# Kernel tuning notes

Hardware: AMD Instinct MI355X
Metric: run time of the kernel (lower is better)

Reference implementation:

```python
import jax, jax.numpy as jnp
import numpy as np

N_EMBD = 1024
N_HEAD = 16
R = 16
SCALING = 1.0 / 16.0  # loralib default lora_alpha=1, scaling = alpha/r


def lora_linear(x, W, b, A, B):
    # loralib: y = x @ W.T + b + (x @ A.T) @ B.T * scaling
    return x @ W.T + b + (x @ A.T) @ B.T * SCALING


def setup_inputs() -> dict:
    key = jax.random.key(0)
    ks = jax.random.split(key, 16)
    B, T, S, C = 8, 1024, 256, N_EMBD
    std = 0.02
    return {
        "x": jax.random.normal(ks[0], (B, T, C), jnp.float32),
        "feature": jax.random.normal(ks[1], (B, S, C), jnp.float32),
        # c_attn (q projection)
        "Wq": jax.random.normal(ks[2], (C, C), jnp.float32) * std,
        "bq": jnp.zeros((C,), jnp.float32),
        "Aq": jax.random.normal(ks[3], (R, C), jnp.float32) * std,
        "Bq": jnp.zeros((C, R), jnp.float32),
        # feature_attn (kv projection)
        "Wf": jax.random.normal(ks[4], (2 * C, C), jnp.float32) * std,
        "bf": jnp.zeros((2 * C,), jnp.float32),
        "Af": jax.random.normal(ks[5], (R, C), jnp.float32) * std,
        "Bf": jnp.zeros((2 * C, R), jnp.float32),
        # c_proj
        "Wp": jax.random.normal(ks[6], (C, C), jnp.float32) * std,
        "bp": jnp.zeros((C,), jnp.float32),
        "Ap": jax.random.normal(ks[7], (R, C), jnp.float32) * std,
        "Bp": jnp.zeros((C, R), jnp.float32),
    }


def reference(x, feature, Wq, bq, Aq, Bq, Wf, bf, Af, Bf, Wp, bp, Ap, Bp):
    Bsz, T, C = x.shape
    S = feature.shape[1]
    H = N_HEAD
    D = C // H

    q = lora_linear(x, Wq, bq, Aq, Bq).reshape(Bsz, T, H, D).transpose(0, 2, 1, 3)
    kv = lora_linear(feature, Wf, bf, Af, Bf)
    k, v = kv[..., :C], kv[..., C:]
    k = k.reshape(Bsz, S, H, D).transpose(0, 2, 1, 3)
    v = v.reshape(Bsz, S, H, D).transpose(0, 2, 1, 3)

    att = jnp.einsum("bhtd,bhsd->bhts", q, k) * (1.0 / np.sqrt(D))
    mask = jnp.tril(jnp.ones((T, S), bool))  # bias[:, :, :T, :S]
    att = jnp.where(mask, att, -jnp.inf)
    att = jax.nn.softmax(att, axis=-1)

    y = jnp.einsum("bhts,bhsd->bhtd", att, v)
    y = y.transpose(0, 2, 1, 3).reshape(Bsz, T, C)
    return lora_linear(y, Wp, bp, Ap, Bp)
```

## Files before the change

kernel.cpp:

```cpp
#include <hip/hip_runtime.h>
#include <hip/hip_bf16.h>
#include <stdint.h>
#include <stddef.h>

typedef __hip_bfloat16 bf16;
typedef __attribute__((ext_vector_type(8))) short short8;
typedef __attribute__((ext_vector_type(4))) float floatx4;

__device__ __forceinline__ void async_load16(const bf16* g, bf16* l) {
#if defined(__has_builtin) && __has_builtin(__builtin_amdgcn_global_load_lds)
  __builtin_amdgcn_global_load_lds((__attribute__((address_space(1))) void*)g,
                                   (__attribute__((address_space(3))) void*)l,
                                   16, 0, 0);
#else
  *(short8*)l = *(const short8*)g;
#endif
}

__device__ __forceinline__ int wave_detect_f32(const unsigned short* __restrict__ xr) {
  const int lane = threadIdx.x & 63;
  const unsigned short u = xr[lane];
  const int e = (u >> 7) & 0xFF;
  const unsigned long long m = __ballot(e >= 0x93);
  return (__popcll(m) > 5) ? 1 : 0;
}

__device__ __forceinline__ float ldf(const void* p, int i, int flg) {
  return flg ? ((const float*)p)[i] : __bfloat162float(((const bf16*)p)[i]);
}

struct PrepArgs {
  const void *x, *ft, *bq, *bf, *bp;
  const void *Wq, *Aq, *Bq, *Wf, *Af, *Bf, *Wp, *Ap, *Bp;
  bf16 *cx, *cft, *cbq, *cbf, *cbp, *weffq, *wefff, *weffp;
};

__device__ __forceinline__ void canon4(const void* src, bf16* dst, int i4, int flg) {
  if (flg) {
    const float4 v = ((const float4*)src)[i4];
    dst[i4 * 4 + 0] = __float2bfloat16(v.x);
    dst[i4 * 4 + 1] = __float2bfloat16(v.y);
    dst[i4 * 4 + 2] = __float2bfloat16(v.z);
    dst[i4 * 4 + 3] = __float2bfloat16(v.w);
  } else {
    ((uint2*)dst)[i4] = ((const uint2*)src)[i4];
  }
}

__device__ __forceinline__ void weff1(const void* W, const void* Bm, const void* Am,
                                      bf16* dst, int idx, int flg) {
  const int n = idx >> 10, k = idx & 1023;
  float acc = 0.f;
#pragma unroll
  for (int r = 0; r < 16; ++r)
    acc += ldf(Bm, n * 16 + r, flg) * ldf(Am, r * 1024 + k, flg);
  dst[idx] = __float2bfloat16(ldf(W, idx, flg) + 0.0625f * acc);
}

__global__ __launch_bounds__(256) void prep_kernel(PrepArgs a) {
  const int flg = wave_detect_f32((const unsigned short*)a.x);
  const int bid = blockIdx.x, tid = threadIdx.x;
  if (bid < 8192) {
    canon4(a.x, a.cx, bid * 256 + tid, flg);
  } else if (bid < 10240) {
    canon4(a.ft, a.cft, (bid - 8192) * 256 + tid, flg);
  } else if (bid < 10241) {
    canon4(a.bq, a.cbq, tid, flg);
  } else if (bid < 10243) {
    canon4(a.bf, a.cbf, (bid - 10241) * 256 + tid, flg);
  } else if (bid < 10244) {
    canon4(a.bp, a.cbp, tid, flg);
  } else if (bid < 14340) {
    weff1(a.Wq, a.Bq, a.Aq, a.weffq, (bid - 10244) * 256 + tid, flg);
  } else if (bid < 22532) {
    weff1(a.Wf, a.Bf, a.Af, a.wefff, (bid - 14340) * 256 + tid, flg);
  } else {
    weff1(a.Wp, a.Bp, a.Ap, a.weffp, (bid - 22532) * 256 + tid, flg);
  }
}

__global__ __launch_bounds__(256) void gemm_qkv(
    const bf16* __restrict__ cx, const bf16* __restrict__ cft,
    const bf16* __restrict__ weffq, const bf16* __restrict__ wefff,
    const bf16* __restrict__ cbq, const bf16* __restrict__ cbf,
    bf16* __restrict__ qws, bf16* __restrict__ kws, bf16* __restrict__ vtws) {
  __shared__ __align__(16) bf16 sA[128 * 32];
  __shared__ __align__(16) bf16 sB[128 * 32];
  const int bid = blockIdx.x, tid = threadIdx.x;
  const int K = 1024;
  int mode, bm, bn;
  const bf16 *A, *Bt, *bias;
  if (bid < 512) {
    mode = 0; A = cx; Bt = weffq; bias = cbq;
    bm = (((bid & 7) << 3) | ((bid >> 3) & 7)) * 128;
    bn = (bid >> 6) * 128;
  } else {
    const int b2 = bid - 512;
    mode = 1; A = cft; Bt = wefff; bias = cbf;
    bm = (((b2 & 7) << 1) | ((b2 >> 3) & 1)) * 128;
    bn = (b2 >> 4) * 128;
  }
  const int srow = tid >> 2;
  const int scol = ((tid & 3) ^ (srow & 3)) << 3;
  const bf16* ga0 = A + (size_t)(bm + srow) * K + scol;
  const bf16* ga1 = ga0 + (size_t)64 * K;
  const bf16* gb0 = Bt + (size_t)(bn + srow) * K + scol;
  const bf16* gb1 = gb0 + (size_t)64 * K;
  bf16* lA0 = sA + tid * 8;
  bf16* lA1 = sA + 2048 + tid * 8;
  bf16* lB0 = sB + tid * 8;
  bf16* lB1 = sB + 2048 + tid * 8;
  const int wave = tid >> 6, lane = tid & 63;
  const int wm = (wave >> 1) << 6, wn = (wave & 1) << 6;
  const int lrow = lane & 15, quad = lane >> 4;
  const int swz = ((quad ^ (lrow & 3)) << 3);

  const floatx4 zero4 = {0.f, 0.f, 0.f, 0.f};
  floatx4 acc[4][4];
#pragma unroll
  for (int i = 0; i < 4; ++i)
#pragma unroll
    for (int j = 0; j < 4; ++j) acc[i][j] = zero4;

  for (int k0 = 0; k0 < K; k0 += 32) {
    async_load16(ga0, lA0);
    async_load16(ga1, lA1);
    async_load16(gb0, lB0);
    async_load16(gb1, lB1);
    ga0 += 32; ga1 += 32; gb0 += 32; gb1 += 32;
    __syncthreads();
    short8 af[4], bfr[4];
#pragma unroll
    for (int i = 0; i < 4; ++i) {
      af[i]  = *(const short8*)(sA + (wm + i * 16 + lrow) * 32 + swz);
      bfr[i] = *(const short8*)(sB + (wn + i * 16 + lrow) * 32 + swz);
    }
#pragma unroll
    for (int i = 0; i < 4; ++i)
#pragma unroll
      for (int j = 0; j < 4; ++j)
        acc[i][j] = __builtin_amdgcn_mfma_f32_16x16x32_bf16(af[i], bfr[j], acc[i][j], 0, 0, 0);
    __syncthreads();
  }

#pragma unroll
  for (int i = 0; i < 4; ++i) {
    const int mbase = bm + wm + i * 16 + quad * 4;
#pragma unroll
    for (int j = 0; j < 4; ++j) {
      const int n = bn + wn + j * 16 + lrow;
      const float bv = __bfloat162float(bias[n]);
#pragma unroll
      for (int r = 0; r < 4; ++r) {
        const int m = mbase + r;
        const bf16 hval = __float2bfloat16(acc[i][j][r] + bv);
        if (mode == 0) {
          const int b = m >> 10, t = m & 1023, hh = n >> 6, d = n & 63;
          qws[(((size_t)(b * 16 + hh)) * 1024 + t) * 64 + d] = hval;
        } else {
          const int b = m >> 8, s = m & 255;
          if (n < 1024) {
            const int hh = n >> 6, d = n & 63;
            kws[(((size_t)(b * 16 + hh)) * 256 + s) * 64 + d] = hval;
          } else {
            const int nn = n - 1024, hh = nn >> 6, d = nn & 63;
            vtws[(((size_t)(b * 16 + hh)) * 64 + d) * 256 + s] = hval;
          }
        }
      }
    }
  }
}

__global__ __launch_bounds__(256) void gemm_out(
    const bf16* __restrict__ A, const bf16* __restrict__ Bt,
    const bf16* __restrict__ bias, void* __restrict__ out0,
    const unsigned short* __restrict__ xraw) {
  __shared__ __align__(16) bf16 sA[128 * 32];
  __shared__ __align__(16) bf16 sB[128 * 32];
  const int bid = blockIdx.x, tid = threadIdx.x;
  const int K = 1024, N = 1024;
  const int bm = (((bid & 7) << 3) | ((bid >> 3) & 7)) * 128;
  const int bn = (bid >> 6) * 128;
  const int srow = tid >> 2;
  const int scol = ((tid & 3) ^ (srow & 3)) << 3;
  const bf16* ga0 = A + (size_t)(bm + srow) * K + scol;
  const bf16* ga1 = ga0 + (size_t)64 * K;
  const bf16* gb0 = Bt + (size_t)(bn + srow) * K + scol;
  const bf16* gb1 = gb0 + (size_t)64 * K;
  bf16* lA0 = sA + tid * 8;
  bf16* lA1 = sA + 2048 + tid * 8;
  bf16* lB0 = sB + tid * 8;
  bf16* lB1 = sB + 2048 + tid * 8;
  const int wave = tid >> 6, lane = tid & 63;
  const int wm = (wave >> 1) << 6, wn = (wave & 1) << 6;
  const int lrow = lane & 15, quad = lane >> 4;
  const int swz = ((quad ^ (lrow & 3)) << 3);

  const floatx4 zero4 = {0.f, 0.f, 0.f, 0.f};
  floatx4 acc[4][4];
#pragma unroll
  for (int i = 0; i < 4; ++i)
#pragma unroll
    for (int j = 0; j < 4; ++j) acc[i][j] = zero4;

  for (int k0 = 0; k0 < K; k0 += 32) {
    async_load16(ga0, lA0);
    async_load16(ga1, lA1);
    async_load16(gb0, lB0);
    async_load16(gb1, lB1);
    ga0 += 32; ga1 += 32; gb0 += 32; gb1 += 32;
    __syncthreads();
    short8 af[4], bfr[4];
#pragma unroll
    for (int i = 0; i < 4; ++i) {
      af[i]  = *(const short8*)(sA + (wm + i * 16 + lrow) * 32 + swz);
      bfr[i] = *(const short8*)(sB + (wn + i * 16 + lrow) * 32 + swz);
    }
#pragma unroll
    for (int i = 0; i < 4; ++i)
#pragma unroll
      for (int j = 0; j < 4; ++j)
        acc[i][j] = __builtin_amdgcn_mfma_f32_16x16x32_bf16(af[i], bfr[j], acc[i][j], 0, 0, 0);
    __syncthreads();
  }

  const int flg = wave_detect_f32(xraw);
#pragma unroll
  for (int i = 0; i < 4; ++i) {
    const int mbase = bm + wm + i * 16 + quad * 4;
#pragma unroll
    for (int j = 0; j < 4; ++j) {
      const int n = bn + wn + j * 16 + lrow;
      const float bv = __bfloat162float(bias[n]);
#pragma unroll
      for (int r = 0; r < 4; ++r) {
        const int m = mbase + r;
        const float fval = acc[i][j][r] + bv;
        const size_t idx = (size_t)m * N + n;
        if (flg) ((float*)out0)[idx] = fval;
        else     ((bf16*)out0)[idx] = __float2bfloat16(fval);
      }
    }
  }
}

#define SKP 72
#define SVP 264
__global__ __launch_bounds__(512, 2) void attn_kernel(
    const bf16* __restrict__ qws, const bf16* __restrict__ kws,
    const bf16* __restrict__ vtws, bf16* __restrict__ yws) {
  const int b = blockIdx.z, h = blockIdx.y, qc = blockIdx.x;
  const int bh = b * 16 + h;
  __shared__ __align__(16) bf16 sK[256 * SKP];
  __shared__ __align__(16) bf16 sVt[64 * SVP];
  __shared__ __align__(16) bf16 sP[8][16 * SVP];
  const int tid = threadIdx.x, wave = tid >> 6, lane = tid & 63;
  const int lrow = lane & 15, quad = lane >> 4;
  const bf16* kg = kws + (size_t)bh * (256 * 64);
  const bf16* vg = vtws + (size_t)bh * (64 * 256);
#pragma unroll
  for (int i = 0; i < 4; ++i) {
    const int idx = i * 512 + tid;
    const int kr = idx >> 3, kc = (idx & 7) * 8;
    *(short8*)(sK + kr * SKP + kc) = *(const short8*)(kg + kr * 64 + kc);
    const int vr = idx >> 5, vc = (idx & 31) * 8;
    *(short8*)(sVt + vr * SVP + vc) = *(const short8*)(vg + vr * 256 + vc);
  }
  __syncthreads();
  bf16* sPw = sP[wave];
  const floatx4 zero4 = {0.f, 0.f, 0.f, 0.f};
  const float kscale = 0.18033688011112042f;

  for (int st = 0; st < 4; ++st) {
    const int t0 = qc * 512 + wave * 64 + st * 16;
    const bf16* qrow = qws + ((size_t)bh * 1024 + t0 + lrow) * 64;
    const short8 aq0 = *(const short8*)(qrow + quad * 8);
    const short8 aq1 = *(const short8*)(qrow + 32 + quad * 8);
    floatx4 sc[16];
#pragma unroll
    for (int nt = 0; nt < 16; ++nt) {
      floatx4 c = zero4;
      c = __builtin_amdgcn_mfma_f32_16x16x32_bf16(
          aq0, *(const short8*)(sK + (nt * 16 + lrow) * SKP + quad * 8), c, 0, 0, 0);
      c = __builtin_amdgcn_mfma_f32_16x16x32_bf16(
          aq1, *(const short8*)(sK + (nt * 16 + lrow) * SKP + 32 + quad * 8), c, 0, 0, 0);
      sc[nt] = c;
    }
    float sum[4] = {0.f, 0.f, 0.f, 0.f};
#pragma unroll
    for (int nt = 0; nt < 16; ++nt) {
      const int s = nt * 16 + lrow;
#pragma unroll
      for (int r = 0; r < 4; ++r) {
        const int t = t0 + quad * 4 + r;
        const float p = (s <= t) ? exp2f(sc[nt][r] * kscale) : 0.f;
        sum[r] += p;
        sPw[(quad * 4 + r) * SVP + nt * 16 + lrow] = __float2bfloat16(p);
      }
    }
#pragma unroll
    for (int r = 0; r < 4; ++r) {
      sum[r] += __shfl_xor(sum[r], 1, 16);
      sum[r] += __shfl_xor(sum[r], 2, 16);
      sum[r] += __shfl_xor(sum[r], 4, 16);
      sum[r] += __shfl_xor(sum[r], 8, 16);
    }
    asm volatile("s_waitcnt lgkmcnt(0)" ::: "memory");
    floatx4 ya[4];
#pragma unroll
    for (int nt = 0; nt < 4; ++nt) ya[nt] = zero4;
#pragma unroll
    for (int ks = 0; ks < 8; ++ks) {
      const short8 ap = *(const short8*)(sPw + lrow * SVP + ks * 32 + quad * 8);
#pragma unroll
      for (int nt = 0; nt < 4; ++nt)
        ya[nt] = __builtin_amdgcn_mfma_f32_16x16x32_bf16(
            ap, *(const short8*)(sVt + (nt * 16 + lrow) * SVP + ks * 32 + quad * 8),
            ya[nt], 0, 0, 0);
    }
#pragma unroll
    for (int r = 0; r < 4; ++r) {
      const float rl = 1.f / sum[r];
      const int t = t0 + quad * 4 + r;
#pragma unroll
      for (int nt = 0; nt < 4; ++nt)
        yws[((size_t)b * 1024 + t) * 1024 + h * 64 + nt * 16 + lrow] =
            __float2bfloat16(ya[nt][r] * rl);
    }
  }
}

extern "C" void kernel_launch(void* const* d_in, const int* in_sizes, int n_in,
                              void* d_out, int out_size, void* d_ws, size_t ws_size,
                              hipStream_t stream) {
  char* p = (char*)d_ws;
  bf16* cbq   = (bf16*)p;     p += 4096;
  bf16* cbf   = (bf16*)p;     p += 8192;
  bf16* cbp   = (bf16*)p;     p += 4096;
  bf16* weffq = (bf16*)p;     p += (size_t)1024 * 1024 * 2;
  bf16* wefff = (bf16*)p;     p += (size_t)2048 * 1024 * 2;
  bf16* weffp = (bf16*)p;     p += (size_t)1024 * 1024 * 2;
  bf16* qws   = (bf16*)p;     p += (size_t)8 * 16 * 1024 * 64 * 2;
  bf16* kws   = (bf16*)p;     p += (size_t)8 * 16 * 256 * 64 * 2;
  bf16* vtws  = (bf16*)p;     p += (size_t)8 * 16 * 64 * 256 * 2;
  bf16* cft   = (bf16*)p;     p += (size_t)8 * 256 * 1024 * 2;
  bf16* cx    = (bf16*)p;     p += (size_t)8 * 1024 * 1024 * 2;
  bf16* yws   = cx;
  const size_t required = (size_t)(p - (char*)d_ws);
  if (ws_size < required) return;

  PrepArgs pa;
  pa.x = d_in[0]; pa.ft = d_in[1];
  pa.bq = d_in[3]; pa.bf = d_in[7]; pa.bp = d_in[11];
  pa.Wq = d_in[2];  pa.Aq = d_in[4];  pa.Bq = d_in[5];
  pa.Wf = d_in[6];  pa.Af = d_in[8];  pa.Bf = d_in[9];
  pa.Wp = d_in[10]; pa.Ap = d_in[12]; pa.Bp = d_in[13];
  pa.cx = cx; pa.cft = cft; pa.cbq = cbq; pa.cbf = cbf; pa.cbp = cbp;
  pa.weffq = weffq; pa.wefff = wefff; pa.weffp = weffp;
  prep_kernel<<<26628, 256, 0, stream>>>(pa);

  gemm_qkv<<<768, 256, 0, stream>>>(cx, cft, weffq, wefff, cbq, cbf, qws, kws, vtws);
  attn_kernel<<<dim3(2, 16, 8), 512, 0, stream>>>(qws, kws, vtws, yws);
  gemm_out<<<512, 256, 0, stream>>>(yws, weffp, cbp, d_out, (const unsigned short*)d_in[0]);
}
```

Baseline: 229.3 us.

## Double-buffer LDS tiles in QKV and output GEMMs with a single barrier

Both GEMM kernels now keep two LDS buffers per operand. The next K-tile's async global-to-LDS loads are issued right after the barrier, so they overlap with the MFMA work on the current tile, and the trailing __syncthreads per iteration is dropped. The XOR swizzle on LDS columns is also removed, so fragment reads use plain quad offsets. That may bring back LDS bank conflicts, and LDS use per block doubles, which can reduce occupancy.

Measured after the change: 237.5 us. 1.04x slower.

```diff
diff --git a/kernel.cpp b/kernel.cpp
--- a/kernel.cpp
+++ b/kernel.cpp
@@ -84,8 +84,8 @@
     const bf16* __restrict__ weffq, const bf16* __restrict__ wefff,
     const bf16* __restrict__ cbq, const bf16* __restrict__ cbf,
     bf16* __restrict__ qws, bf16* __restrict__ kws, bf16* __restrict__ vtws) {
-  __shared__ __align__(16) bf16 sA[128 * 32];
-  __shared__ __align__(16) bf16 sB[128 * 32];
+  __shared__ __align__(16) bf16 sA[2][128 * 32];
+  __shared__ __align__(16) bf16 sB[2][128 * 32];
   const int bid = blockIdx.x, tid = threadIdx.x;
   const int K = 1024;
   int mode, bm, bn;
@@ -100,20 +100,14 @@
     bm = (((b2 & 7) << 1) | ((b2 >> 3) & 1)) * 128;
     bn = (b2 >> 4) * 128;
   }
-  const int srow = tid >> 2;
-  const int scol = ((tid & 3) ^ (srow & 3)) << 3;
+  const int srow = tid >> 2, scol = (tid & 3) << 3;
   const bf16* ga0 = A + (size_t)(bm + srow) * K + scol;
   const bf16* ga1 = ga0 + (size_t)64 * K;
   const bf16* gb0 = Bt + (size_t)(bn + srow) * K + scol;
   const bf16* gb1 = gb0 + (size_t)64 * K;
-  bf16* lA0 = sA + tid * 8;
-  bf16* lA1 = sA + 2048 + tid * 8;
-  bf16* lB0 = sB + tid * 8;
-  bf16* lB1 = sB + 2048 + tid * 8;
   const int wave = tid >> 6, lane = tid & 63;
   const int wm = (wave >> 1) << 6, wn = (wave & 1) << 6;
   const int lrow = lane & 15, quad = lane >> 4;
-  const int swz = ((quad ^ (lrow & 3)) << 3);
 
   const floatx4 zero4 = {0.f, 0.f, 0.f, 0.f};
   floatx4 acc[4][4];
@@ -122,25 +116,35 @@
 #pragma unroll
     for (int j = 0; j < 4; ++j) acc[i][j] = zero4;
 
+  async_load16(ga0, &sA[0][tid * 8]);
+  async_load16(ga1, &sA[0][2048 + tid * 8]);
+  async_load16(gb0, &sB[0][tid * 8]);
+  async_load16(gb1, &sB[0][2048 + tid * 8]);
+  ga0 += 32; ga1 += 32; gb0 += 32; gb1 += 32;
+
+  int cur = 0;
   for (int k0 = 0; k0 < K; k0 += 32) {
-    async_load16(ga0, lA0);
-    async_load16(ga1, lA1);
-    async_load16(gb0, lB0);
-    async_load16(gb1, lB1);
-    ga0 += 32; ga1 += 32; gb0 += 32; gb1 += 32;
     __syncthreads();
+    if (k0 + 32 < K) {
+      const int nxt = cur ^ 1;
+      async_load16(ga0, &sA[nxt][tid * 8]);
+      async_load16(ga1, &sA[nxt][2048 + tid * 8]);
+      async_load16(gb0, &sB[nxt][tid * 8]);
+      async_load16(gb1, &sB[nxt][2048 + tid * 8]);
+      ga0 += 32; ga1 += 32; gb0 += 32; gb1 += 32;
+    }
     short8 af[4], bfr[4];
 #pragma unroll
     for (int i = 0; i < 4; ++i) {
-      af[i]  = *(const short8*)(sA + (wm + i * 16 + lrow) * 32 + swz);
-      bfr[i] = *(const short8*)(sB + (wn + i * 16 + lrow) * 32 + swz);
+      af[i]  = *(const short8*)(&sA[cur][(wm + i * 16 + lrow) * 32 + quad * 8]);
+      bfr[i] = *(const short8*)(&sB[cur][(wn + i * 16 + lrow) * 32 + quad * 8]);
     }
 #pragma unroll
     for (int i = 0; i < 4; ++i)
 #pragma unroll
       for (int j = 0; j < 4; ++j)
         acc[i][j] = __builtin_amdgcn_mfma_f32_16x16x32_bf16(af[i], bfr[j], acc[i][j], 0, 0, 0);
-    __syncthreads();
+    cur ^= 1;
   }
 
 #pragma unroll
@@ -176,26 +180,20 @@
     const bf16* __restrict__ A, const bf16* __restrict__ Bt,
     const bf16* __restrict__ bias, void* __restrict__ out0,
     const unsigned short* __restrict__ xraw) {
-  __shared__ __align__(16) bf16 sA[128 * 32];
-  __shared__ __align__(16) bf16 sB[128 * 32];
+  __shared__ __align__(16) bf16 sA[2][128 * 32];
+  __shared__ __align__(16) bf16 sB[2][128 * 32];
   const int bid = blockIdx.x, tid = threadIdx.x;
   const int K = 1024, N = 1024;
   const int bm = (((bid & 7) << 3) | ((bid >> 3) & 7)) * 128;
   const int bn = (bid >> 6) * 128;
-  const int srow = tid >> 2;
-  const int scol = ((tid & 3) ^ (srow & 3)) << 3;
+  const int srow = tid >> 2, scol = (tid & 3) << 3;
   const bf16* ga0 = A + (size_t)(bm + srow) * K + scol;
   const bf16* ga1 = ga0 + (size_t)64 * K;
   const bf16* gb0 = Bt + (size_t)(bn + srow) * K + scol;
   const bf16* gb1 = gb0 + (size_t)64 * K;
-  bf16* lA0 = sA + tid * 8;
-  bf16* lA1 = sA + 2048 + tid * 8;
-  bf16* lB0 = sB + tid * 8;
-  bf16* lB1 = sB + 2048 + tid * 8;
   const int wave = tid >> 6, lane = tid & 63;
   const int wm = (wave >> 1) << 6, wn = (wave & 1) << 6;
   const int lrow = lane & 15, quad = lane >> 4;
-  const int swz = ((quad ^ (lrow & 3)) << 3);
 
   const floatx4 zero4 = {0.f, 0.f, 0.f, 0.f};
   floatx4 acc[4][4];
@@ -204,25 +202,35 @@
 #pragma unroll
     for (int j = 0; j < 4; ++j) acc[i][j] = zero4;
 
+  async_load16(ga0, &sA[0][tid * 8]);
+  async_load16(ga1, &sA[0][2048 + tid * 8]);
+  async_load16(gb0, &sB[0][tid * 8]);
+  async_load16(gb1, &sB[0][2048 + tid * 8]);
+  ga0 += 32; ga1 += 32; gb0 += 32; gb1 += 32;
+
+  int cur = 0;
   for (int k0 = 0; k0 < K; k0 += 32) {
-    async_load16(ga0, lA0);
-    async_load16(ga1, lA1);
-    async_load16(gb0, lB0);
-    async_load16(gb1, lB1);
-    ga0 += 32; ga1 += 32; gb0 += 32; gb1 += 32;
     __syncthreads();
+    if (k0 + 32 < K) {
+      const int nxt = cur ^ 1;
+      async_load16(ga0, &sA[nxt][tid * 8]);
+      async_load16(ga1, &sA[nxt][2048 + tid * 8]);
+      async_load16(gb0, &sB[nxt][tid * 8]);
+      async_load16(gb1, &sB[nxt][2048 + tid * 8]);
+      ga0 += 32; ga1 += 32; gb0 += 32; gb1 += 32;
+    }
     short8 af[4], bfr[4];
 #pragma unroll
     for (int i = 0; i < 4; ++i) {
-      af[i]  = *(const short8*)(sA + (wm + i * 16 + lrow) * 32 + swz);
-      bfr[i] = *(const short8*)(sB + (wn + i * 16 + lrow) * 32 + swz);
+      af[i]  = *(const short8*)(&sA[cur][(wm + i * 16 + lrow) * 32 + quad * 8]);
+      bfr[i] = *(const short8*)(&sB[cur][(wn + i * 16 + lrow) * 32 + quad * 8]);
     }
 #pragma unroll
     for (int i = 0; i < 4; ++i)
 #pragma unroll
       for (int j = 0; j < 4; ++j)
         acc[i][j] = __builtin_amdgcn_mfma_f32_16x16x32_bf16(af[i], bfr[j], acc[i][j], 0, 0, 0);
-    __syncthreads();
+    cur ^= 1;
   }
 
   const int flg = wave_detect_f32(xraw);
```
